# Kernel optimization log

Hardware: AMD Instinct MI355X
Metric: run time of the kernel (lower is better)

The kernel has to match this reference:

```python
import jax, jax.numpy as jnp
import numpy as np

C = 1.0            # curvature
MIN_NORM = 1e-15   # hgcn min_norm
PROJ_EPS = 4e-3    # hgcn PoincareBall float32 boundary eps
N, D, E = 100000, 128, 1600000


def _artanh(x):
    # hgcn Artanh clamps input away from +-1 for stability
    return jnp.arctanh(jnp.clip(x, -1.0 + 1e-5, 1.0 - 1e-5))


def logmap0(p, c):
    sqrt_c = c ** 0.5
    p_norm = jnp.maximum(jnp.linalg.norm(p, axis=-1, keepdims=True), MIN_NORM)
    return p * _artanh(sqrt_c * p_norm) / (sqrt_c * p_norm)


def expmap0(u, c):
    sqrt_c = c ** 0.5
    u_norm = jnp.maximum(jnp.linalg.norm(u, axis=-1, keepdims=True), MIN_NORM)
    return jnp.tanh(sqrt_c * u_norm) * u / (sqrt_c * u_norm)


def proj(x, c):
    norm = jnp.maximum(jnp.linalg.norm(x, axis=-1, keepdims=True), MIN_NORM)
    maxnorm = (1.0 - PROJ_EPS) / (c ** 0.5)
    return jnp.where(norm > maxnorm, x / norm * maxnorm, x)


def setup_inputs() -> dict:
    key = jax.random.key(0)
    k1, k2, k3, k4 = jax.random.split(key, 4)
    # node features on the Poincare ball (small tangent vectors -> exp -> proj)
    x = proj(0.05 * jax.random.normal(k1, (N, D), dtype=jnp.float32), C)
    rows = jax.random.randint(k2, (E,), 0, N, dtype=jnp.int32)   # dst nodes
    cols = jax.random.randint(k3, (E,), 0, N, dtype=jnp.int32)   # src nodes
    # positive edge weights, roughly row-normalized (avg degree 16)
    vals = jax.random.uniform(k4, (E,), dtype=jnp.float32) / 16.0
    return {"x": x, "rows": rows, "cols": cols, "vals": vals}


def reference(x, rows, cols, vals):
    # x_tangent = logmap0(x)
    x_tangent = logmap0(x, C)                         # [N, D]
    # support_t = spmm(adj, x_tangent): gather src features, weight, scatter-add to dst
    msgs = vals[:, None] * x_tangent[cols]            # [E, D]
    support_t = jax.ops.segment_sum(msgs, rows, num_segments=N)  # [N, D]
    # output = proj(expmap0(support_t))
    return proj(expmap0(support_t, C), C)
```

## Files before the change

kernel.cpp:

```cpp
#include <hip/hip_runtime.h>
#include <hip/hip_fp16.h>
#include <math.h>

#define DIM 128
#define MAXNORM (1.0f - 4e-3f)
#define SUPR 128
#define EPB 4096
#define CAP 48
#define CSTRIDE 32
#define RBLK 512
#define FCAP 64
#define MAXNSB 2048

__device__ __forceinline__ float wave_reduce_sum(float v) {
    #pragma unroll
    for (int off = 32; off > 0; off >>= 1)
        v += __shfl_xor(v, off, 64);
    return v;
}

__device__ __forceinline__ unsigned pack_h2(float a, float b) {
    unsigned lo = (unsigned)__half_as_ushort(__float2half_rn(a));
    unsigned hi = (unsigned)__half_as_ushort(__float2half_rn(b));
    return lo | (hi << 16);
}

__device__ __forceinline__ float tanh_fast(float x) {
    float e = __expf(2.0f * x);
    return 1.0f - 2.0f / (e + 1.0f);
}

__global__ void fused_xt_partA(const float* __restrict__ x,
                               unsigned* __restrict__ xt, int n,
                               const int* __restrict__ rows,
                               const int* __restrict__ cols,
                               const float* __restrict__ vals,
                               int* __restrict__ scur, uint2* __restrict__ sup,
                               int E, int NSB, int CAPS, int nA) {
    __shared__ int locCur[MAXNSB];
    int tid = threadIdx.x;
    if ((int)blockIdx.x < nA) {
        int base = blockIdx.x * EPB;
        int er[8]; int ec[8]; float ev[8];
        #pragma unroll
        for (int k = 0; k < 8; k++) {
            int e = base + k * RBLK + tid;
            bool ok = e < E;
            er[k] = ok ? rows[e] : -1;
            ec[k] = ok ? cols[e] : 0;
            ev[k] = ok ? vals[e] : 0.f;
        }
        for (int i = tid; i < NSB; i += RBLK) locCur[i] = 0;
        __syncthreads();
        #pragma unroll
        for (int k = 0; k < 8; k++)
            if (er[k] >= 0) atomicAdd(&locCur[er[k] >> 7], 1);
        __syncthreads();
        for (int i = tid; i < NSB; i += RBLK) {
            int a = locCur[i];
            locCur[i] = a ? atomicAdd(&scur[i], a) : 0;
        }
        __syncthreads();
        #pragma unroll
        for (int k = 0; k < 8; k++) {
            if (er[k] >= 0) {
                int r = er[k];
                int s = r >> 7;
                unsigned hw = (unsigned)__half_as_ushort(__float2half(ev[k])) & 0x7fffu;
                unsigned rx = (hw << 17) | (unsigned)ec[k];
                int slot = atomicAdd(&locCur[s], 1);
                if (slot < CAPS)
                    sup[(size_t)s * CAPS + slot] = make_uint2(rx, (unsigned)r);
            }
        }
        return;
    }
    int wave = (int)(((blockIdx.x - nA) * RBLK + tid) >> 6);
    int lane = tid & 63;
    if (wave >= n) return;
    const float2* xr = (const float2*)(x + (size_t)wave * DIM);
    float2 v = xr[lane];
    float ss = wave_reduce_sum(v.x * v.x + v.y * v.y);
    float norm = sqrtf(ss);
    float t = fminf(norm, 1.0f - 1e-5f);
    float at = 0.5f * logf((1.0f + t) / (1.0f - t));
    float f = at / fmaxf(norm, 1e-15f);
    xt[(size_t)wave * 64 + lane] = pack_h2(v.x * f, v.y * f);
}

__global__ void __launch_bounds__(RBLK, 8)
partB_gather_kernel(const unsigned* __restrict__ xt,
                    const int* __restrict__ scur,
                    const uint2* __restrict__ sup,
                    float* __restrict__ out, int n, int CAPS) {
    __shared__ unsigned ell[SUPR * CAP];
    __shared__ int cnt[SUPR];
    int s = blockIdx.x;
    int tid = threadIdx.x;
    int row0 = s * SUPR;
    int rowsInB = n - row0; if (rowsInB > SUPR) rowsInB = SUPR;
    for (int i = tid; i < SUPR; i += RBLK) cnt[i] = 0;
    __syncthreads();
    int total = scur[s]; if (total > CAPS) total = CAPS;
    const uint2* src = sup + (size_t)s * CAPS;
    for (int i = tid; i < total; i += RBLK) {
        uint2 rec = src[i];
        int lr = (int)(rec.y & (SUPR - 1));
        int p = atomicAdd(&cnt[lr], 1);
        if (p < CAP) ell[lr * CAP + p] = rec.x;
    }
    __syncthreads();
    if (tid < SUPR) {
        int d = cnt[tid]; if (d > CAP) d = CAP;
        int dp = (d + 7) & ~7; if (dp > CAP) dp = CAP;
        for (int q = d; q < dp; ++q) ell[tid * CAP + q] = 0;
    }
    __syncthreads();
    int wv = tid >> 6, lane = tid & 63;
    unsigned lane4 = (unsigned)(lane << 2);
    for (int lr = wv; lr < rowsInB; lr += RBLK / 64) {
        int deg = cnt[lr]; if (deg > CAP) deg = CAP;
        float ax = 0.f, ay = 0.f;
        const unsigned* erow = &ell[lr * CAP];
        for (int j = 0; j < deg; j += 8) {
            uint4 qa = *(const uint4*)(erow + j);
            uint4 qb = *(const uint4*)(erow + j + 4);
            unsigned pk[8] = {qa.x, qa.y, qa.z, qa.w, qb.x, qb.y, qb.z, qb.w};
            __half2 u[8];
            #pragma unroll
            for (int k = 0; k < 8; k++) {
                unsigned voff = ((pk[k] & 0x1ffffu) << 8) + lane4;
                u[k] = *(const __half2*)((const char*)xt + voff);
            }
            #pragma unroll
            for (int k = 0; k < 8; k++) {
                float w = __half2float(__ushort_as_half((unsigned short)(pk[k] >> 17)));
                ax = fmaf(w, __low2float(u[k]), ax);
                ay = fmaf(w, __high2float(u[k]), ay);
            }
        }
        float ssum = wave_reduce_sum(ax * ax + ay * ay);
        float n0 = fmaxf(sqrtf(ssum), 1e-15f);
        float th = tanh_fast(n0);
        float f = (th > MAXNORM) ? (MAXNORM / n0) : (th / n0);
        float2* o = (float2*)(out + (size_t)(row0 + lr) * DIM);
        o[lane] = make_float2(ax * f, ay * f);
    }
}

__global__ void xt_kernel(const float* __restrict__ x,
                          unsigned* __restrict__ xt, int n) {
    int wave = (int)((blockIdx.x * blockDim.x + threadIdx.x) >> 6);
    int lane = threadIdx.x & 63;
    if (wave >= n) return;
    const float2* xr = (const float2*)(x + (size_t)wave * DIM);
    float2 v = xr[lane];
    float ss = wave_reduce_sum(v.x * v.x + v.y * v.y);
    float norm = sqrtf(ss);
    float t = fminf(norm, 1.0f - 1e-5f);
    float at = 0.5f * logf((1.0f + t) / (1.0f - t));
    float f = at / fmaxf(norm, 1e-15f);
    xt[(size_t)wave * 64 + lane] = pack_h2(v.x * f, v.y * f);
}

__global__ void scatter_ell_kernel(const int* __restrict__ rows,
                                   const int* __restrict__ cols,
                                   const float* __restrict__ vals,
                                   int* __restrict__ cur,
                                   unsigned* __restrict__ ell, int E) {
    int e = blockIdx.x * blockDim.x + threadIdx.x;
    if (e >= E) return;
    int r = rows[e];
    unsigned hb = (unsigned)__half_as_ushort(__float2half(vals[e])) & 0x7fffu;
    unsigned pk = ((unsigned)cols[e] << 15) | hb;
    int pos = atomicAdd(&cur[(size_t)r * CSTRIDE], 1);
    if (pos < FCAP) ell[(size_t)r * FCAP + pos] = pk;
}

__global__ void gather_ell_kernel(const unsigned* __restrict__ xt,
                                  const unsigned* __restrict__ ell,
                                  const int* __restrict__ cur,
                                  float* __restrict__ out, int n) {
    int wave = (int)((blockIdx.x * blockDim.x + threadIdx.x) >> 6);
    int lane = threadIdx.x & 63;
    if (wave >= n) return;
    const __half2* xt2 = (const __half2*)xt;
    int deg = cur[(size_t)wave * CSTRIDE];
    if (deg > FCAP) deg = FCAP;
    unsigned pl = 0;
    if (lane < deg) pl = ell[(size_t)wave * FCAP + lane];
    float2 acc = make_float2(0.f, 0.f);
    for (int j = 0; j < deg; j += 8) {
        float w[8]; __half2 u[8]; int c[8];
        #pragma unroll
        for (int k = 0; k < 8; k++) {
            int idx = j + k;
            bool ok = idx < deg;
            unsigned p = __shfl(pl, ok ? idx : 0);
            c[k] = (int)(p >> 15);
            w[k] = ok ? __half2float(__ushort_as_half((unsigned short)(p & 0x7fffu))) : 0.f;
        }
        #pragma unroll
        for (int k = 0; k < 8; k++)
            u[k] = xt2[(size_t)c[k] * 64 + lane];
        #pragma unroll
        for (int k = 0; k < 8; k++) {
            acc.x = fmaf(w[k], __low2float(u[k]), acc.x);
            acc.y = fmaf(w[k], __high2float(u[k]), acc.y);
        }
    }
    float ss = wave_reduce_sum(acc.x * acc.x + acc.y * acc.y);
    float n0 = fmaxf(sqrtf(ss), 1e-15f);
    float th = tanhf(n0);
    float f = (th > MAXNORM) ? (MAXNORM / n0) : (th / n0);
    float2* o = (float2*)(out + (size_t)wave * DIM);
    o[lane] = make_float2(acc.x * f, acc.y * f);
}

__global__ void tangent_kernel(const float* __restrict__ x,
                               float* __restrict__ xt, int n) {
    int wave = (int)((blockIdx.x * blockDim.x + threadIdx.x) >> 6);
    int lane = threadIdx.x & 63;
    if (wave >= n) return;
    const float2* xr = (const float2*)(x + (size_t)wave * DIM);
    float2 v = xr[lane];
    float ss = wave_reduce_sum(v.x * v.x + v.y * v.y);
    float norm = sqrtf(ss);
    float t = fminf(norm, 1.0f - 1e-5f);
    float at = 0.5f * logf((1.0f + t) / (1.0f - t));
    float factor = at / fmaxf(norm, 1e-15f);
    float2* o = (float2*)(xt + (size_t)wave * DIM);
    o[lane] = make_float2(v.x * factor, v.y * factor);
}

__global__ void scatter_kernel(const float* __restrict__ xt,
                               const int* __restrict__ rows,
                               const int* __restrict__ cols,
                               const float* __restrict__ vals,
                               float* __restrict__ out, int E) {
    long gid = (long)blockIdx.x * blockDim.x + threadIdx.x;
    int e = (int)(gid >> 5);
    int lane = (int)(gid & 31);
    if (e >= E) return;
    int r = rows[e];
    int c = cols[e];
    float w = vals[e];
    const float4* src = (const float4*)(xt + (size_t)c * DIM);
    float4 v = src[lane];
    float* dst = out + (size_t)r * DIM + lane * 4;
    unsafeAtomicAdd(dst + 0, v.x * w);
    unsafeAtomicAdd(dst + 1, v.y * w);
    unsafeAtomicAdd(dst + 2, v.z * w);
    unsafeAtomicAdd(dst + 3, v.w * w);
}

__global__ void finalize_kernel(float* __restrict__ out, int n) {
    int wave = (int)((blockIdx.x * blockDim.x + threadIdx.x) >> 6);
    int lane = threadIdx.x & 63;
    if (wave >= n) return;
    float2* p = (float2*)(out + (size_t)wave * DIM);
    float2 v = p[lane];
    float ss = wave_reduce_sum(v.x * v.x + v.y * v.y);
    float n0 = fmaxf(sqrtf(ss), 1e-15f);
    float th = tanhf(n0);
    float factor = (th > MAXNORM) ? (MAXNORM / n0) : (th / n0);
    p[lane] = make_float2(v.x * factor, v.y * factor);
}

extern "C" void kernel_launch(void* const* d_in, const int* in_sizes, int n_in,
                              void* d_out, int out_size, void* d_ws, size_t ws_size,
                              hipStream_t stream) {
    const float* x    = (const float*)d_in[0];
    const int*   rows = (const int*)d_in[1];
    const int*   cols = (const int*)d_in[2];
    const float* vals = (const float*)d_in[3];
    float* out = (float*)d_out;

    int n = in_sizes[0] / DIM;
    int E = in_sizes[1];
    int NSB = (n + SUPR - 1) / SUPR;

    auto align256 = [](size_t b) { return (b + 255) & ~(size_t)255; };

    size_t xt_b = align256((size_t)n * 64 * 4);

    double smean = (NSB > 0) ? (double)E / (double)NSB : 0.0;
    int caps = ((int)(smean + 8.0 * sqrt(smean + 1.0)) + 31) & ~31;

    size_t sup_b  = align256((size_t)NSB * (size_t)caps * 8);
    size_t meta_b = align256((size_t)NSB * 4);
    size_t need   = xt_b + sup_b + meta_b;

    if (n > 0 && n <= (1 << 17) && NSB <= MAXNSB && need <= ws_size) {
        unsigned* xt_h = (unsigned*)d_ws;
        uint2*    sup  = (uint2*)((char*)d_ws + xt_b);
        int*      scur = (int*)((char*)d_ws + xt_b + sup_b);

        hipMemsetAsync(scur, 0, (size_t)NSB * 4, stream);
        int nA  = (E > 0) ? (E + EPB - 1) / EPB : 0;
        int nXt = (n * 64 + RBLK - 1) / RBLK;
        fused_xt_partA<<<nA + nXt, RBLK, 0, stream>>>(x, xt_h, n, rows, cols, vals,
                                                      scur, sup, E, NSB, caps, nA);
        partB_gather_kernel<<<NSB, RBLK, 0, stream>>>(xt_h, scur, sup, out, n, caps);
        return;
    }

    size_t ell_b = align256((size_t)n * FCAP * 4);
    size_t cur_b = align256((size_t)n * CSTRIDE * 4);
    if (n <= (1 << 17) && xt_b + ell_b + cur_b <= ws_size) {
        unsigned* xt_h = (unsigned*)d_ws;
        unsigned* ell  = (unsigned*)((char*)d_ws + xt_b);
        int*      cur  = (int*)((char*)d_ws + xt_b + ell_b);
        xt_kernel<<<(n + 3) / 4, 256, 0, stream>>>(x, xt_h, n);
        hipMemsetAsync(cur, 0, (size_t)n * CSTRIDE * 4, stream);
        scatter_ell_kernel<<<(E + 255) / 256, 256, 0, stream>>>(rows, cols, vals, cur, ell, E);
        gather_ell_kernel<<<(n + 3) / 4, 256, 0, stream>>>(xt_h, ell, cur, out, n);
        return;
    }

    float* xtf = (float*)d_in[0];
    size_t xtb = (size_t)n * DIM * sizeof(float);
    if (ws_size >= xtb) xtf = (float*)d_ws;
    tangent_kernel<<<(n + 3) / 4, 256, 0, stream>>>(x, xtf, n);
    hipMemsetAsync(d_out, 0, (size_t)n * DIM * sizeof(float), stream);
    long threads = (long)E * 32;
    scatter_kernel<<<(int)((threads + 255) / 256), 256, 0, stream>>>(xtf, rows, cols, vals, out, E);
    finalize_kernel<<<(n + 3) / 4, 256, 0, stream>>>(out, n);
}
```

Measured before the change: 208.5 us.

## Process two rows per wave with 8-byte half-feature loads in gather and xt

Each wavefront now handles two rows at once, using 32 lanes per row with 4 features per lane, in both the tangent-map conversion and the gather phase. Gather loads become 8-byte uint2 reads of fp16 features and stores become float4, and reductions use a 32-lane shuffle. Padding zeros are extended to the max degree of the row pair so both halves iterate the same trip count. This halves the number of wave iterations and widens memory transactions, at the cost of extra work on zero-padded edges when the paired rows' degrees differ. The xt phase also switches logf to __logf.

```diff
diff --git a/kernel.cpp b/kernel.cpp
--- a/kernel.cpp
+++ b/kernel.cpp
@@ -15,6 +15,13 @@
 __device__ __forceinline__ float wave_reduce_sum(float v) {
     #pragma unroll
     for (int off = 32; off > 0; off >>= 1)
+        v += __shfl_xor(v, off, 64);
+    return v;
+}
+
+__device__ __forceinline__ float half_reduce_sum(float v) {
+    #pragma unroll
+    for (int off = 16; off > 0; off >>= 1)
         v += __shfl_xor(v, off, 64);
     return v;
 }
@@ -75,17 +82,19 @@
         }
         return;
     }
-    int wave = (int)(((blockIdx.x - nA) * RBLK + tid) >> 6);
-    int lane = tid & 63;
-    if (wave >= n) return;
-    const float2* xr = (const float2*)(x + (size_t)wave * DIM);
-    float2 v = xr[lane];
-    float ss = wave_reduce_sum(v.x * v.x + v.y * v.y);
+    int wv = tid >> 6, lane = tid & 63;
+    int half = lane >> 5, ld = lane & 31;
+    int row = ((int)blockIdx.x - nA) * 16 + wv * 2 + half;
+    if (row >= n) return;
+    const float4* xr = (const float4*)(x + (size_t)row * DIM);
+    float4 v = xr[ld];
+    float ss = half_reduce_sum(v.x * v.x + v.y * v.y + v.z * v.z + v.w * v.w);
     float norm = sqrtf(ss);
     float t = fminf(norm, 1.0f - 1e-5f);
-    float at = 0.5f * logf((1.0f + t) / (1.0f - t));
+    float at = 0.5f * __logf((1.0f + t) / (1.0f - t));
     float f = at / fmaxf(norm, 1e-15f);
-    xt[(size_t)wave * 64 + lane] = pack_h2(v.x * f, v.y * f);
+    uint2 o = make_uint2(pack_h2(v.x * f, v.y * f), pack_h2(v.z * f, v.w * f));
+    *(uint2*)((char*)xt + ((size_t)row << 8) + (ld << 3)) = o;
 }
 
 __global__ void __launch_bounds__(RBLK, 8)
@@ -111,40 +120,52 @@
     }
     __syncthreads();
     if (tid < SUPR) {
-        int d = cnt[tid]; if (d > CAP) d = CAP;
-        int dp = (d + 7) & ~7; if (dp > CAP) dp = CAP;
-        for (int q = d; q < dp; ++q) ell[tid * CAP + q] = 0;
+        int d0 = cnt[tid];     if (d0 > CAP) d0 = CAP;
+        int d1 = cnt[tid ^ 1]; if (d1 > CAP) d1 = CAP;
+        int dm = d0 > d1 ? d0 : d1;
+        int dp = (dm + 7) & ~7; if (dp > CAP) dp = CAP;
+        for (int q = d0; q < dp; ++q) ell[tid * CAP + q] = 0;
     }
     __syncthreads();
     int wv = tid >> 6, lane = tid & 63;
-    unsigned lane4 = (unsigned)(lane << 2);
-    for (int lr = wv; lr < rowsInB; lr += RBLK / 64) {
-        int deg = cnt[lr]; if (deg > CAP) deg = CAP;
-        float ax = 0.f, ay = 0.f;
+    int half = lane >> 5, ld = lane & 31;
+    unsigned lane8 = (unsigned)(ld << 3);
+    for (int pair = wv; pair < SUPR / 2; pair += 8) {
+        int lr0 = pair * 2;
+        if (lr0 >= rowsInB) break;
+        int lr = lr0 + half;
+        int d0 = cnt[lr0];     if (d0 > CAP) d0 = CAP;
+        int d1 = cnt[lr0 + 1]; if (d1 > CAP) d1 = CAP;
+        int tc = ((d0 > d1 ? d0 : d1) + 7) & ~7; if (tc > CAP) tc = CAP;
+        float ax = 0.f, ay = 0.f, az = 0.f, aw = 0.f;
         const unsigned* erow = &ell[lr * CAP];
-        for (int j = 0; j < deg; j += 8) {
+        for (int j = 0; j < tc; j += 8) {
             uint4 qa = *(const uint4*)(erow + j);
             uint4 qb = *(const uint4*)(erow + j + 4);
             unsigned pk[8] = {qa.x, qa.y, qa.z, qa.w, qb.x, qb.y, qb.z, qb.w};
-            __half2 u[8];
+            uint2 u[8];
             #pragma unroll
             for (int k = 0; k < 8; k++) {
-                unsigned voff = ((pk[k] & 0x1ffffu) << 8) + lane4;
-                u[k] = *(const __half2*)((const char*)xt + voff);
+                unsigned voff = ((pk[k] & 0x1ffffu) << 8) + lane8;
+                u[k] = *(const uint2*)((const char*)xt + voff);
             }
             #pragma unroll
             for (int k = 0; k < 8; k++) {
                 float w = __half2float(__ushort_as_half((unsigned short)(pk[k] >> 17)));
-                ax = fmaf(w, __low2float(u[k]), ax);
-                ay = fmaf(w, __high2float(u[k]), ay);
+                ax = fmaf(w, __half2float(__ushort_as_half((unsigned short)(u[k].x & 0xffffu))), ax);
+                ay = fmaf(w, __half2float(__ushort_as_half((unsigned short)(u[k].x >> 16))), ay);
+                az = fmaf(w, __half2float(__ushort_as_half((unsigned short)(u[k].y & 0xffffu))), az);
+                aw = fmaf(w, __half2float(__ushort_as_half((unsigned short)(u[k].y >> 16))), aw);
             }
         }
-        float ssum = wave_reduce_sum(ax * ax + ay * ay);
+        float ssum = half_reduce_sum(ax * ax + ay * ay + az * az + aw * aw);
         float n0 = fmaxf(sqrtf(ssum), 1e-15f);
         float th = tanh_fast(n0);
         float f = (th > MAXNORM) ? (MAXNORM / n0) : (th / n0);
-        float2* o = (float2*)(out + (size_t)(row0 + lr) * DIM);
-        o[lane] = make_float2(ax * f, ay * f);
+        if (lr < rowsInB) {
+            float4* o = (float4*)(out + (size_t)(row0 + lr) * DIM);
+            o[ld] = make_float4(ax * f, ay * f, az * f, aw * f);
+        }
     }
 }
 
@@ -298,7 +319,7 @@
 
         hipMemsetAsync(scur, 0, (size_t)NSB * 4, stream);
         int nA  = (E > 0) ? (E + EPB - 1) / EPB : 0;
-        int nXt = (n * 64 + RBLK - 1) / RBLK;
+        int nXt = (n + 15) / 16;
         fused_xt_partA<<<nA + nXt, RBLK, 0, stream>>>(x, xt_h, n, rows, cols, vals,
                                                       scur, sup, E, NSB, caps, nA);
         partB_gather_kernel<<<NSB, RBLK, 0, stream>>>(xt_h, scur, sup, out, n, caps);
```

Result: faster. 202.9 us (-2.7%).
